# Kernel tuning notes

Measured on AMD Instinct MI355X. Metric: run time of the kernel, lower is better.

## Reference

```python
import jax, jax.numpy as jnp
import numpy as np

B, NX, NY, CIN = 4, 128, 128, 64
D, H = 64, 8  # out_channels, nhead
EPS = 1e-5


def setup_inputs() -> dict:
    key = jax.random.key(0)
    ks = jax.random.split(key, 12)
    s_in = 1.0 / np.sqrt(CIN)
    s_hd = 1.0 / np.sqrt(H * D)
    return {
        "v": jax.random.normal(ks[0], (B, NX, NY, CIN), jnp.float32),
        "Wq_w": jax.random.uniform(ks[1], (CIN, H * D), jnp.float32, -s_in, s_in),
        "Wq_b": jax.random.uniform(ks[2], (H * D,), jnp.float32, -s_in, s_in),
        "Wk_w": jax.random.uniform(ks[3], (CIN, H * D), jnp.float32, -s_in, s_in),
        "Wk_b": jax.random.uniform(ks[4], (H * D,), jnp.float32, -s_in, s_in),
        "Wv_w": jax.random.uniform(ks[5], (CIN, H * D), jnp.float32, -s_in, s_in),
        "Wv_b": jax.random.uniform(ks[6], (H * D,), jnp.float32, -s_in, s_in),
        "lnq_g": jnp.ones((H, D), jnp.float32),
        "lnq_b": jnp.zeros((H, D), jnp.float32),
        "lnk_g": jnp.ones((H, D), jnp.float32),
        "lnk_b": jnp.zeros((H, D), jnp.float32),
        "Wo_w": jax.random.uniform(ks[7], (H * D, D), jnp.float32, -s_hd, s_hd),
        "Wo_b": jax.random.uniform(ks[8], (D,), jnp.float32, -s_hd, s_hd),
    }


def _layernorm(x, gamma, beta):
    # x: [b,h,n,d]; gamma/beta: [h,d] (per-head params)
    mu = jnp.mean(x, axis=-1, keepdims=True)
    var = jnp.mean(jnp.square(x - mu), axis=-1, keepdims=True)
    xn = (x - mu) * jax.lax.rsqrt(var + EPS)
    return xn * gamma[None, :, None, :] + beta[None, :, None, :]


def reference(v, Wq_w, Wq_b, Wk_w, Wk_b, Wv_w, Wv_b,
              lnq_g, lnq_b, lnk_g, lnk_b, Wo_w, Wo_b):
    b, nx, ny, _ = v.shape
    n = nx * ny
    vf = v.reshape(b, n, -1)  # [b, n, cin]
    # QKV projections -> [b, h, n, d]
    def proj(w, bias):
        y = vf @ w + bias  # [b, n, h*d]
        return y.reshape(b, n, H, D).transpose(0, 2, 1, 3)
    Q = _layernorm(proj(Wq_w, Wq_b), lnq_g, lnq_b)
    K = _layernorm(proj(Wk_w, Wk_b), lnk_g, lnk_b)
    V = proj(Wv_w, Wv_b)
    # Non-softmax linear attention: (Q K^T) V == Q (K^T V); use O(n d^2) form
    kv = jnp.einsum('bhnd,bhne->bhde', K, V)      # [b,h,d,d]
    attn = jnp.einsum('bhmd,bhde->bhme', Q, kv)   # [b,h,n,d]
    attn = attn.transpose(0, 2, 1, 3).reshape(b, n, H * D)
    out = (attn @ Wo_w + Wo_b) / n
    return out.reshape(b, nx, ny, D)
```

## Files before the change

kernel.cpp:

```cpp
#include <hip/hip_runtime.h>
#include <hip/hip_bf16.h>

typedef __attribute__((ext_vector_type(8))) short bhalf8;
typedef __attribute__((ext_vector_type(4))) float f32x4;

#define MFMA_BF16 __builtin_amdgcn_mfma_f32_16x16x32_bf16

namespace {

constexpr int   NPIX  = 16384;
constexpr float EPSV  = 1e-5f;
constexpr float INV64 = 1.0f / 64.0f;
constexpr float INV_N = 1.0f / 16384.0f;

constexpr int KV1_OFF   = 0;
constexpr int T_OFF     = 131072;
constexpr int VSUM_OFF  = 131072 + 2048;
constexpr int CBETA_OFF = 131072 + 2048 + 256;
constexpr int FZERO_CNT = 131072 + 2048 + 256 + 256;

__device__ __host__ __forceinline__ unsigned short f2bf(float f) {
    unsigned int u = __builtin_bit_cast(unsigned int, f);
    u += 0x7fffu + ((u >> 16) & 1u);
    return (unsigned short)(u >> 16);
}

union B8 { bhalf8 v; unsigned int u[4]; ushort4 s4[2]; };

__device__ __forceinline__ unsigned int pk2(float a, float b) {
    union { __hip_bfloat162 h; unsigned int u; } x;
    x.h = __float22bfloat162_rn(float2{a, b});
    return x.u;
}

__global__ void k0_vsum(const float* __restrict__ v, float* __restrict__ vsum)
{
    const int blk = blockIdx.x, b = blockIdx.y, t = threadIdx.x;
    const int c4 = t & 15, p = t >> 4;
    float4 a = make_float4(0.f, 0.f, 0.f, 0.f);
    const float* base = v + ((size_t)b * NPIX + blk * 128) * 64 + c4 * 4;
#pragma unroll
    for (int i = 0; i < 8; ++i) {
        const float4 x = *reinterpret_cast<const float4*>(base + (size_t)(p * 8 + i) * 64);
        a.x += x.x; a.y += x.y; a.z += x.z; a.w += x.w;
    }
    __shared__ float4 red[16][16];
    red[p][c4] = a;
    __syncthreads();
    if (t < 16) {
        float4 s = red[0][t];
#pragma unroll
        for (int i = 1; i < 16; ++i) {
            const float4 x = red[i][t];
            s.x += x.x; s.y += x.y; s.z += x.z; s.w += x.w;
        }
        atomicAdd(vsum + b * 64 + t * 4 + 0, s.x);
        atomicAdd(vsum + b * 64 + t * 4 + 1, s.y);
        atomicAdd(vsum + b * 64 + t * 4 + 2, s.z);
        atomicAdd(vsum + b * 64 + t * 4 + 3, s.w);
    }
}

__global__ void kpack(const float* __restrict__ Wk, const float* __restrict__ Wv,
                      const float* __restrict__ Wq,
                      unsigned short* __restrict__ wkpk, unsigned short* __restrict__ wvpk,
                      unsigned short* __restrict__ wqpk, unsigned short* __restrict__ wksumb)
{
    const int w = blockIdx.x >> 3, h = blockIdx.x & 7, t = threadIdx.x;
    const float* W = (w == 0) ? Wk : (w == 1) ? Wv : Wq;
    unsigned short* dst = (w == 0) ? wkpk : (w == 1) ? wvpk : wqpk;

#pragma unroll
    for (int i = 0; i < 2; ++i) {
        const int f = t * 2 + i;
        const int nt = (f >> 7) & 3, ks = (f >> 6) & 1, l = f & 63;
        const int g = l >> 4, m = l & 15;
        ushort4 o0, o1;
        unsigned short tmp[8];
#pragma unroll
        for (int j = 0; j < 8; ++j)
            tmp[j] = f2bf(W[(size_t)(32 * ks + 8 * g + j) * 512 + h * 64 + 16 * nt + m]);
        o0 = make_ushort4(tmp[0], tmp[1], tmp[2], tmp[3]);
        o1 = make_ushort4(tmp[4], tmp[5], tmp[6], tmp[7]);
        unsigned short* d = dst + ((size_t)((h * 4 + nt) * 2 + ks)) * 512 + l * 8;
        *reinterpret_cast<ushort4*>(d)     = o0;
        *reinterpret_cast<ushort4*>(d + 4) = o1;
    }
    if (w == 0 && t < 64) {
        float s = 0.f;
        const float* row = Wk + (size_t)t * 512 + h * 64;
#pragma unroll
        for (int d = 0; d < 64; ++d) s += row[d];
        wksumb[h * 64 + t] = f2bf(s);
    }
}

__global__ __launch_bounds__(256, 2)
void k1_kv(const float* __restrict__ v,
           const unsigned short* __restrict__ wkpk, const unsigned short* __restrict__ wvpk,
           const unsigned short* __restrict__ wksumb,
           const float* __restrict__ bk, const float* __restrict__ bv,
           float* __restrict__ kv1, float* __restrict__ tG)
{
    const int ch = blockIdx.x, h = blockIdx.y, b = blockIdx.z;
    const int t = threadIdx.x, w = t >> 6, l = t & 63, g = l >> 4, m16 = l & 15;

    bhalf8 wkB[4][2], wvB[4][2], wks[2];
#pragma unroll
    for (int nt = 0; nt < 4; ++nt)
#pragma unroll
      for (int ks = 0; ks < 2; ++ks) {
          wkB[nt][ks] = *reinterpret_cast<const bhalf8*>(
              wkpk + ((size_t)((h * 4 + nt) * 2 + ks)) * 512 + l * 8);
          wvB[nt][ks] = *reinterpret_cast<const bhalf8*>(
              wvpk + ((size_t)((h * 4 + nt) * 2 + ks)) * 512 + l * 8);
      }
#pragma unroll
    for (int ks = 0; ks < 2; ++ks)
        wks[ks] = *reinterpret_cast<const bhalf8*>(wksumb + h * 64 + 32 * ks + 8 * g);

    float bksum;
    {
        float bl = bk[h * 64 + l];
#pragma unroll
        for (int m = 1; m < 64; m <<= 1) bl += __shfl_xor(bl, m, 64);
        bksum = bl;
    }
    float bkv[4], bvv[4];
#pragma unroll
    for (int nt = 0; nt < 4; ++nt) {
        bkv[nt] = bk[h * 64 + 16 * nt + m16];
        bvv[nt] = bv[h * 64 + 16 * nt + m16];
    }

    f32x4 kv[4][4];
#pragma unroll
    for (int i = 0; i < 4; ++i)
#pragma unroll
      for (int j = 0; j < 4; ++j) kv[i][j] = f32x4{0.f, 0.f, 0.f, 0.f};
    float tl[4] = {0.f, 0.f, 0.f, 0.f};

    const float* vw = v + ((size_t)b * NPIX + ch * 1024 + w * 256) * 64;

    for (int s = 0; s < 8; ++s) {
        B8 vA[2][2];
#pragma unroll
        for (int mt = 0; mt < 2; ++mt)
#pragma unroll
          for (int ks = 0; ks < 2; ++ks) {
              const float* src = vw + (size_t)(s * 32 + 16 * mt + m16) * 64 + 32 * ks + 8 * g;
              const float4 a = *reinterpret_cast<const float4*>(src);
              const float4 c = *reinterpret_cast<const float4*>(src + 4);
              vA[mt][ks].u[0] = pk2(a.x, a.y); vA[mt][ks].u[1] = pk2(a.z, a.w);
              vA[mt][ks].u[2] = pk2(c.x, c.y); vA[mt][ks].u[3] = pk2(c.z, c.w);
          }

        f32x4 kq[2][4];
#pragma unroll
        for (int mt = 0; mt < 2; ++mt)
#pragma unroll
          for (int nt = 0; nt < 4; ++nt) {
              f32x4 a = {0.f, 0.f, 0.f, 0.f};
              a = MFMA_BF16(vA[mt][0].v, wkB[nt][0], a, 0, 0, 0);
              a = MFMA_BF16(vA[mt][1].v, wkB[nt][1], a, 0, 0, 0);
#pragma unroll
              for (int q = 0; q < 4; ++q) a[q] += bkv[nt];
              kq[mt][nt] = a;
          }
        f32x4 st[2];
#pragma unroll
        for (int mt = 0; mt < 2; ++mt) {
            f32x4 a = {0.f, 0.f, 0.f, 0.f};
            a = MFMA_BF16(vA[mt][0].v, wks[0], a, 0, 0, 0);
            a = MFMA_BF16(vA[mt][1].v, wks[1], a, 0, 0, 0);
            st[mt] = a;
        }
        f32x4 s2p[2];
#pragma unroll
        for (int mt = 0; mt < 2; ++mt) {
#pragma unroll
            for (int q = 0; q < 4; ++q) {
                float acc = kq[mt][0][q] * kq[mt][0][q];
                acc = fmaf(kq[mt][1][q], kq[mt][1][q], acc);
                acc = fmaf(kq[mt][2][q], kq[mt][2][q], acc);
                acc = fmaf(kq[mt][3][q], kq[mt][3][q], acc);
                s2p[mt][q] = acc;
            }
        }
#pragma unroll
        for (int mt = 0; mt < 2; ++mt)
#pragma unroll
          for (int q = 0; q < 4; ++q) {
              float x = s2p[mt][q];
              x += __shfl_xor(x, 1, 64);
              x += __shfl_xor(x, 2, 64);
              x += __shfl_xor(x, 4, 64);
              x += __shfl_xor(x, 8, 64);
              s2p[mt][q] = x;
          }
        f32x4 rsv[2], cmu[2];
#pragma unroll
        for (int mt = 0; mt < 2; ++mt)
#pragma unroll
          for (int q = 0; q < 4; ++q) {
              const float mu  = (st[mt][q] + bksum) * INV64;
              const float var = s2p[mt][q] * INV64 - mu * mu;
              const float rs  = rsqrtf(fmaxf(var, 0.f) + EPSV);
              rsv[mt][q] = rs;
              cmu[mt][q] = mu * rs;
          }
        B8 ka[4];
#pragma unroll
        for (int MT = 0; MT < 4; ++MT) {
            ka[MT].u[0] = pk2(kq[0][MT][0] * rsv[0][0], kq[0][MT][1] * rsv[0][1]);
            ka[MT].u[1] = pk2(kq[0][MT][2] * rsv[0][2], kq[0][MT][3] * rsv[0][3]);
            ka[MT].u[2] = pk2(kq[1][MT][0] * rsv[1][0], kq[1][MT][1] * rsv[1][1]);
            ka[MT].u[3] = pk2(kq[1][MT][2] * rsv[1][2], kq[1][MT][3] * rsv[1][3]);
        }
        f32x4 vq[2][4];
#pragma unroll
        for (int mt = 0; mt < 2; ++mt)
#pragma unroll
          for (int nt = 0; nt < 4; ++nt) {
              f32x4 a = {0.f, 0.f, 0.f, 0.f};
              a = MFMA_BF16(vA[mt][0].v, wvB[nt][0], a, 0, 0, 0);
              a = MFMA_BF16(vA[mt][1].v, wvB[nt][1], a, 0, 0, 0);
#pragma unroll
              for (int q = 0; q < 4; ++q) a[q] += bvv[nt];
              vq[mt][nt] = a;
          }
#pragma unroll
        for (int nt = 0; nt < 4; ++nt) {
            float acc = tl[nt];
#pragma unroll
            for (int mt = 0; mt < 2; ++mt)
#pragma unroll
              for (int q = 0; q < 4; ++q)
                  acc = fmaf(cmu[mt][q], vq[mt][nt][q], acc);
            tl[nt] = acc;
        }
        B8 vb[4];
#pragma unroll
        for (int NT = 0; NT < 4; ++NT) {
            vb[NT].u[0] = pk2(vq[0][NT][0], vq[0][NT][1]);
            vb[NT].u[1] = pk2(vq[0][NT][2], vq[0][NT][3]);
            vb[NT].u[2] = pk2(vq[1][NT][0], vq[1][NT][1]);
            vb[NT].u[3] = pk2(vq[1][NT][2], vq[1][NT][3]);
        }
#pragma unroll
        for (int MT = 0; MT < 4; ++MT)
#pragma unroll
          for (int NT = 0; NT < 4; ++NT)
              kv[MT][NT] = MFMA_BF16(ka[MT].v, vb[NT].v, kv[MT][NT], 0, 0, 0);
    }

#pragma unroll
    for (int nt = 0; nt < 4; ++nt) {
        float x = tl[nt];
        x += __shfl_xor(x, 16, 64);
        x += __shfl_xor(x, 32, 64);
        tl[nt] = x;
    }
    if (g == 0) {
        float* td = tG + ((size_t)(b * 8 + h)) * 64;
#pragma unroll
        for (int nt = 0; nt < 4; ++nt) atomicAdd(td + 16 * nt + m16, tl[nt]);
    }

    __shared__ float kvred[4][4096];
    __syncthreads();
#pragma unroll
    for (int MT = 0; MT < 4; ++MT)
#pragma unroll
      for (int NT = 0; NT < 4; ++NT)
#pragma unroll
        for (int q = 0; q < 4; ++q)
            kvred[w][(16 * MT + 4 * g + q) * 64 + 16 * NT + m16] = kv[MT][NT][q];
    __syncthreads();
    float* dstg = kv1 + ((size_t)(b * 8 + h)) * 4096;
#pragma unroll
    for (int i = 0; i < 16; ++i) {
        const int idx = i * 256 + t;
        atomicAdd(dstg + idx,
                  kvred[0][idx] + kvred[1][idx] + kvred[2][idx] + kvred[3][idx]);
    }
}

__global__ void k2_mix(const float* __restrict__ kv1,  const float* __restrict__ tG,
                       const float* __restrict__ vsum,
                       const float* __restrict__ Wv,   const float* __restrict__ bv,
                       const float* __restrict__ lnkg, const float* __restrict__ lnkb,
                       const float* __restrict__ lnqg, const float* __restrict__ lnqb,
                       const float* __restrict__ Wo,   const float* __restrict__ Wob,
                       unsigned short* __restrict__ mpk, float* __restrict__ cbeta)
{
    const int h = blockIdx.x, b = blockIdx.y, t = threadIdx.x;
    __shared__ float kvs[64][65], wos[64][65], mls[64][65], Svs[64], us[64];
    const int r = t >> 2, c0 = (t & 3) * 16;
    const float* kg = kv1 + ((size_t)(b * 8 + h)) * 4096;
    const float* td = tG + ((size_t)(b * 8 + h)) * 64;
#pragma unroll
    for (int i = 0; i < 16; i += 4) {
        const float4 x = *reinterpret_cast<const float4*>(kg + r * 64 + c0 + i);
        kvs[r][c0+i] = x.x; kvs[r][c0+i+1] = x.y; kvs[r][c0+i+2] = x.z; kvs[r][c0+i+3] = x.w;
    }
#pragma unroll
    for (int i = 0; i < 16; i += 4) {
        const float4 x = *reinterpret_cast<const float4*>(Wo + ((size_t)(h * 64) + r) * 64 + c0 + i);
        wos[r][c0+i] = x.x; wos[r][c0+i+1] = x.y; wos[r][c0+i+2] = x.z; wos[r][c0+i+3] = x.w;
    }
    if (t < 64) {
        float s = 16384.f * bv[h * 64 + t];
        for (int cc = 0; cc < 64; ++cc)
            s = fmaf(vsum[b * 64 + cc], Wv[cc * 512 + h * 64 + t], s);
        Svs[t] = s;
    }
    __syncthreads();
    {
        const float gk = lnkg[h * 64 + r], bk2 = lnkb[h * 64 + r];
#pragma unroll
        for (int i = 0; i < 16; ++i) {
            const int e = c0 + i;
            kvs[r][e] = gk * (kvs[r][e] - td[e]) + bk2 * Svs[e];
        }
    }
    __syncthreads();
    if (t < 64) {
        float s = 0.f;
        for (int dd = 0; dd < 64; ++dd) s = fmaf(lnqb[h * 64 + dd], kvs[dd][t], s);
        us[t] = s;
    }
    float mrow[16];
#pragma unroll
    for (int i = 0; i < 16; ++i) mrow[i] = 0.f;
    for (int e2 = 0; e2 < 64; ++e2) {
        const float kr = kvs[r][e2];
#pragma unroll
        for (int i = 0; i < 16; ++i) mrow[i] = fmaf(kr, wos[e2][c0 + i], mrow[i]);
    }
    {
        const float gq = lnqg[h * 64 + r] * INV_N;
#pragma unroll
        for (int i = 0; i < 16; ++i) mls[r][c0 + i] = gq * mrow[i];
    }
    __syncthreads();
    if (t < 64) {
        float s = 0.f;
        for (int e2 = 0; e2 < 64; ++e2) s = fmaf(us[e2], wos[e2][t], s);
        atomicAdd(cbeta + b * 64 + t, s * INV_N);
        if (h == 0) atomicAdd(cbeta + b * 64 + t, Wob[t] * INV_N);
    }
#pragma unroll
    for (int i = 0; i < 2; ++i) {
        const int f = t * 2 + i;
        const int nt = (f >> 7) & 3, ks = (f >> 6) & 1, l = f & 63;
        const int g = l >> 4, m = l & 15;
        unsigned short o[8];
#pragma unroll
        for (int j = 0; j < 8; ++j) {
            const int d = 32 * ks + 16 * (j >> 2) + 4 * g + (j & 3);
            o[j] = f2bf(mls[d][16 * nt + m]);
        }
        unsigned short* dd = mpk + ((size_t)((b * 8 + h) * 8 + nt * 2 + ks)) * 512 + l * 8;
        *reinterpret_cast<ushort4*>(dd)     = make_ushort4(o[0], o[1], o[2], o[3]);
        *reinterpret_cast<ushort4*>(dd + 4) = make_ushort4(o[4], o[5], o[6], o[7]);
    }
}

__global__ __launch_bounds__(256, 2)
void k3_out(const float* __restrict__ v,
            const unsigned short* __restrict__ wqpk, const float* __restrict__ bq,
            const unsigned short* __restrict__ mpk,  const float* __restrict__ cbeta,
            float* __restrict__ out)
{
    const int blk = blockIdx.x, b = blockIdx.y;
    const int t = threadIdx.x, w = t >> 6, l = t & 63, g = l >> 4, m16 = l & 15;
    const size_t px0 = (size_t)b * NPIX + blk * 128 + w * 32;

    B8 vB[2][2];
#pragma unroll
    for (int nt = 0; nt < 2; ++nt)
#pragma unroll
      for (int ks = 0; ks < 2; ++ks) {
          const float* src = v + (px0 + 16 * nt + m16) * 64 + 32 * ks + 8 * g;
          const float4 a = *reinterpret_cast<const float4*>(src);
          const float4 c = *reinterpret_cast<const float4*>(src + 4);
          vB[nt][ks].u[0] = pk2(a.x, a.y); vB[nt][ks].u[1] = pk2(a.z, a.w);
          vB[nt][ks].u[2] = pk2(c.x, c.y); vB[nt][ks].u[3] = pk2(c.z, c.w);
      }
    float cbv[4];
#pragma unroll
    for (int nt = 0; nt < 4; ++nt) cbv[nt] = cbeta[b * 64 + 16 * nt + m16];

    f32x4 outa[2][4];
#pragma unroll
    for (int i = 0; i < 2; ++i)
#pragma unroll
      for (int j = 0; j < 4; ++j) outa[i][j] = f32x4{0.f, 0.f, 0.f, 0.f};

    for (int h = 0; h < 8; ++h) {
        bhalf8 wqA[4][2], mB[2][4];
#pragma unroll
        for (int mt = 0; mt < 4; ++mt)
#pragma unroll
          for (int ks = 0; ks < 2; ++ks)
            wqA[mt][ks] = *reinterpret_cast<const bhalf8*>(
                wqpk + ((size_t)((h * 4 + mt) * 2 + ks)) * 512 + l * 8);
#pragma unroll
        for (int ks = 0; ks < 2; ++ks)
#pragma unroll
          for (int nt = 0; nt < 4; ++nt)
            mB[ks][nt] = *reinterpret_cast<const bhalf8*>(
                mpk + ((size_t)((b * 8 + h) * 8 + nt * 2 + ks)) * 512 + l * 8);
        float4 bq4[4];
#pragma unroll
        for (int mt = 0; mt < 4; ++mt)
            bq4[mt] = *reinterpret_cast<const float4*>(bq + h * 64 + 16 * mt + 4 * g);

        f32x4 qa[4][2];
#pragma unroll
        for (int mt = 0; mt < 4; ++mt)
#pragma unroll
          for (int nt = 0; nt < 2; ++nt) {
              f32x4 a = {0.f, 0.f, 0.f, 0.f};
              a = MFMA_BF16(wqA[mt][0], vB[nt][0].v, a, 0, 0, 0);
              a = MFMA_BF16(wqA[mt][1], vB[nt][1].v, a, 0, 0, 0);
              a[0] += bq4[mt].x; a[1] += bq4[mt].y;
              a[2] += bq4[mt].z; a[3] += bq4[mt].w;
              qa[mt][nt] = a;
          }
        float mu[2], rs[2];
#pragma unroll
        for (int nt = 0; nt < 2; ++nt) {
            float s1 = 0.f, s2 = 0.f;
#pragma unroll
            for (int mt = 0; mt < 4; ++mt)
#pragma unroll
              for (int q = 0; q < 4; ++q) {
                  const float x = qa[mt][nt][q];
                  s1 += x; s2 = fmaf(x, x, s2);
              }
            s1 += __shfl_xor(s1, 16, 64); s1 += __shfl_xor(s1, 32, 64);
            s2 += __shfl_xor(s2, 16, 64); s2 += __shfl_xor(s2, 32, 64);
            mu[nt] = s1 * INV64;
            rs[nt] = rsqrtf(fmaxf(s2 * INV64 - mu[nt] * mu[nt], 0.f) + EPSV);
        }
        B8 ka[2][2];
#pragma unroll
        for (int MT = 0; MT < 2; ++MT)
#pragma unroll
          for (int ks = 0; ks < 2; ++ks) {
              ka[MT][ks].u[0] = pk2((qa[2*ks+0][MT][0] - mu[MT]) * rs[MT],
                                    (qa[2*ks+0][MT][1] - mu[MT]) * rs[MT]);
              ka[MT][ks].u[1] = pk2((qa[2*ks+0][MT][2] - mu[MT]) * rs[MT],
                                    (qa[2*ks+0][MT][3] - mu[MT]) * rs[MT]);
              ka[MT][ks].u[2] = pk2((qa[2*ks+1][MT][0] - mu[MT]) * rs[MT],
                                    (qa[2*ks+1][MT][1] - mu[MT]) * rs[MT]);
              ka[MT][ks].u[3] = pk2((qa[2*ks+1][MT][2] - mu[MT]) * rs[MT],
                                    (qa[2*ks+1][MT][3] - mu[MT]) * rs[MT]);
          }
#pragma unroll
        for (int MT = 0; MT < 2; ++MT)
#pragma unroll
          for (int nt = 0; nt < 4; ++nt) {
              outa[MT][nt] = MFMA_BF16(ka[MT][0].v, mB[0][nt], outa[MT][nt], 0, 0, 0);
              outa[MT][nt] = MFMA_BF16(ka[MT][1].v, mB[1][nt], outa[MT][nt], 0, 0, 0);
          }
    }

#pragma unroll
    for (int MT = 0; MT < 2; ++MT)
#pragma unroll
      for (int q = 0; q < 4; ++q) {
          float* orow = out + (px0 + 16 * MT + 4 * g + q) * 64;
#pragma unroll
          for (int nt = 0; nt < 4; ++nt)
              orow[16 * nt + m16] = outa[MT][nt][q] + cbv[nt];
      }
}

}

extern "C" void kernel_launch(void* const* d_in, const int* in_sizes, int n_in,
                              void* d_out, int out_size, void* d_ws, size_t ws_size,
                              hipStream_t stream)
{
    const float* v     = (const float*)d_in[0];
    const float* Wq_w  = (const float*)d_in[1];
    const float* Wq_b  = (const float*)d_in[2];
    const float* Wk_w  = (const float*)d_in[3];
    const float* Wk_b  = (const float*)d_in[4];
    const float* Wv_w  = (const float*)d_in[5];
    const float* Wv_b  = (const float*)d_in[6];
    const float* lnq_g = (const float*)d_in[7];
    const float* lnq_b = (const float*)d_in[8];
    const float* lnk_g = (const float*)d_in[9];
    const float* lnk_b = (const float*)d_in[10];
    const float* Wo_w  = (const float*)d_in[11];
    const float* Wo_b  = (const float*)d_in[12];
    float* out = (float*)d_out;

    float* wsf   = (float*)d_ws;
    float* kv1   = wsf + KV1_OFF;
    float* tG    = wsf + T_OFF;
    float* vsum  = wsf + VSUM_OFF;
    float* cbeta = wsf + CBETA_OFF;
    unsigned short* base_s = (unsigned short*)(wsf + FZERO_CNT);
    unsigned short* wkpk   = base_s;
    unsigned short* wvpk   = base_s + 32768;
    unsigned short* wqpk   = base_s + 65536;
    unsigned short* wksumb = base_s + 98304;
    unsigned short* mpk    = base_s + 98816;

    hipMemsetAsync(d_ws, 0, (size_t)FZERO_CNT * sizeof(float), stream);
    k0_vsum<<<dim3(128, 4), 256, 0, stream>>>(v, vsum);
    kpack<<<24, 256, 0, stream>>>(Wk_w, Wv_w, Wq_w, wkpk, wvpk, wqpk, wksumb);
    k1_kv<<<dim3(16, 8, 4), 256, 0, stream>>>(v, wkpk, wvpk, wksumb, Wk_b, Wv_b,
                                              kv1, tG);
    k2_mix<<<dim3(8, 4), 256, 0, stream>>>(kv1, tG, vsum, Wv_w, Wv_b,
                                           lnk_g, lnk_b, lnq_g, lnq_b,
                                           Wo_w, Wo_b, mpk, cbeta);
    k3_out<<<dim3(128, 4), 256, 0, stream>>>(v, wqpk, Wq_b, mpk, cbeta, out);
}
```

Baseline: 178.9 us.

## Share v tile across heads in LDS and replace atomics with two-stage reduction

The KV kernel now runs one 512-thread block per (chunk, batch), with each wave handling one head. It converts a 256-pixel tile of v to bf16 once into LDS instead of having every head re-read and re-convert v from global memory. Per-block partial kv/t/sum-of-V tiles are written to a workspace and reduced deterministically by a new reduce kernel plus the mix kernel. This removes the global atomics, the memset and the separate vsum kernel, since the V column sum is now accumulated in the KV pass. The cost is a larger workspace and extra global traffic for the partial tiles, plus one more launch.

```diff
diff --git a/kernel.cpp b/kernel.cpp
--- a/kernel.cpp
+++ b/kernel.cpp
@@ -9,23 +9,19 @@
 namespace {
 
 constexpr int   NPIX  = 16384;
+constexpr int   NCH   = 64;
+constexpr int   TILE  = 66 * 64;
 constexpr float EPSV  = 1e-5f;
 constexpr float INV64 = 1.0f / 64.0f;
 constexpr float INV_N = 1.0f / 16384.0f;
 
-constexpr int KV1_OFF   = 0;
-constexpr int T_OFF     = 131072;
-constexpr int VSUM_OFF  = 131072 + 2048;
-constexpr int CBETA_OFF = 131072 + 2048 + 256;
-constexpr int FZERO_CNT = 131072 + 2048 + 256 + 256;
-
-__device__ __host__ __forceinline__ unsigned short f2bf(float f) {
+__device__ __forceinline__ unsigned short f2bf(float f) {
     unsigned int u = __builtin_bit_cast(unsigned int, f);
     u += 0x7fffu + ((u >> 16) & 1u);
     return (unsigned short)(u >> 16);
 }
 
-union B8 { bhalf8 v; unsigned int u[4]; ushort4 s4[2]; };
+union B8 { bhalf8 v; unsigned int u[4]; };
 
 __device__ __forceinline__ unsigned int pk2(float a, float b) {
     union { __hip_bfloat162 h; unsigned int u; } x;
@@ -33,58 +29,30 @@
     return x.u;
 }
 
-__global__ void k0_vsum(const float* __restrict__ v, float* __restrict__ vsum)
-{
-    const int blk = blockIdx.x, b = blockIdx.y, t = threadIdx.x;
-    const int c4 = t & 15, p = t >> 4;
-    float4 a = make_float4(0.f, 0.f, 0.f, 0.f);
-    const float* base = v + ((size_t)b * NPIX + blk * 128) * 64 + c4 * 4;
-#pragma unroll
-    for (int i = 0; i < 8; ++i) {
-        const float4 x = *reinterpret_cast<const float4*>(base + (size_t)(p * 8 + i) * 64);
-        a.x += x.x; a.y += x.y; a.z += x.z; a.w += x.w;
-    }
-    __shared__ float4 red[16][16];
-    red[p][c4] = a;
-    __syncthreads();
-    if (t < 16) {
-        float4 s = red[0][t];
-#pragma unroll
-        for (int i = 1; i < 16; ++i) {
-            const float4 x = red[i][t];
-            s.x += x.x; s.y += x.y; s.z += x.z; s.w += x.w;
-        }
-        atomicAdd(vsum + b * 64 + t * 4 + 0, s.x);
-        atomicAdd(vsum + b * 64 + t * 4 + 1, s.y);
-        atomicAdd(vsum + b * 64 + t * 4 + 2, s.z);
-        atomicAdd(vsum + b * 64 + t * 4 + 3, s.w);
-    }
-}
-
 __global__ void kpack(const float* __restrict__ Wk, const float* __restrict__ Wv,
                       const float* __restrict__ Wq,
                       unsigned short* __restrict__ wkpk, unsigned short* __restrict__ wvpk,
-                      unsigned short* __restrict__ wqpk, unsigned short* __restrict__ wksumb)
+                      unsigned short* __restrict__ wqpk, unsigned short* __restrict__ wksumb,
+                      float* __restrict__ cbeta)
 {
     const int w = blockIdx.x >> 3, h = blockIdx.x & 7, t = threadIdx.x;
     const float* W = (w == 0) ? Wk : (w == 1) ? Wv : Wq;
     unsigned short* dst = (w == 0) ? wkpk : (w == 1) ? wvpk : wqpk;
 
+    if (blockIdx.x == 0) cbeta[t] = 0.f;
+
 #pragma unroll
     for (int i = 0; i < 2; ++i) {
         const int f = t * 2 + i;
         const int nt = (f >> 7) & 3, ks = (f >> 6) & 1, l = f & 63;
         const int g = l >> 4, m = l & 15;
-        ushort4 o0, o1;
         unsigned short tmp[8];
 #pragma unroll
         for (int j = 0; j < 8; ++j)
             tmp[j] = f2bf(W[(size_t)(32 * ks + 8 * g + j) * 512 + h * 64 + 16 * nt + m]);
-        o0 = make_ushort4(tmp[0], tmp[1], tmp[2], tmp[3]);
-        o1 = make_ushort4(tmp[4], tmp[5], tmp[6], tmp[7]);
         unsigned short* d = dst + ((size_t)((h * 4 + nt) * 2 + ks)) * 512 + l * 8;
-        *reinterpret_cast<ushort4*>(d)     = o0;
-        *reinterpret_cast<ushort4*>(d + 4) = o1;
+        *reinterpret_cast<ushort4*>(d)     = make_ushort4(tmp[0], tmp[1], tmp[2], tmp[3]);
+        *reinterpret_cast<ushort4*>(d + 4) = make_ushort4(tmp[4], tmp[5], tmp[6], tmp[7]);
     }
     if (w == 0 && t < 64) {
         float s = 0.f;
@@ -95,15 +63,30 @@
     }
 }
 
-__global__ __launch_bounds__(256, 2)
-void k1_kv(const float* __restrict__ v,
+__global__ __launch_bounds__(512, 2)
+void ka_kv(const float* __restrict__ v,
            const unsigned short* __restrict__ wkpk, const unsigned short* __restrict__ wvpk,
            const unsigned short* __restrict__ wksumb,
            const float* __restrict__ bk, const float* __restrict__ bv,
-           float* __restrict__ kv1, float* __restrict__ tG)
+           float* __restrict__ part)
 {
-    const int ch = blockIdx.x, h = blockIdx.y, b = blockIdx.z;
-    const int t = threadIdx.x, w = t >> 6, l = t & 63, g = l >> 4, m16 = l & 15;
+    const int ch = blockIdx.x, b = blockIdx.y;
+    const int t = threadIdx.x, h = t >> 6, l = t & 63, g = l >> 4, m16 = l & 15;
+
+    __shared__ uint4 vlds4[2048];
+    unsigned short* vlds = reinterpret_cast<unsigned short*>(vlds4);
+
+    const float* vbase = v + ((size_t)b * NPIX + ch * 256) * 64;
+#pragma unroll
+    for (int i = 0; i < 4; ++i) {
+        const int G = t + 512 * i;
+        const int s = G >> 8, f = (G >> 6) & 3, ll = G & 63;
+        const int mt = f >> 1, ks = f & 1, gg = ll >> 4, mm = ll & 15;
+        const float* src = vbase + (size_t)(s * 32 + 16 * mt + mm) * 64 + 32 * ks + 8 * gg;
+        const float4 a = *reinterpret_cast<const float4*>(src);
+        const float4 c = *reinterpret_cast<const float4*>(src + 4);
+        vlds4[G] = uint4{pk2(a.x, a.y), pk2(a.z, a.w), pk2(c.x, c.y), pk2(c.z, c.w)};
+    }
 
     bhalf8 wkB[4][2], wvB[4][2], wks[2];
 #pragma unroll
@@ -139,21 +122,18 @@
 #pragma unroll
       for (int j = 0; j < 4; ++j) kv[i][j] = f32x4{0.f, 0.f, 0.f, 0.f};
     float tl[4] = {0.f, 0.f, 0.f, 0.f};
-
-    const float* vw = v + ((size_t)b * NPIX + ch * 1024 + w * 256) * 64;
+    float sv[4] = {0.f, 0.f, 0.f, 0.f};
+
+    __syncthreads();
 
     for (int s = 0; s < 8; ++s) {
-        B8 vA[2][2];
+        bhalf8 vA[2][2];
 #pragma unroll
         for (int mt = 0; mt < 2; ++mt)
 #pragma unroll
-          for (int ks = 0; ks < 2; ++ks) {
-              const float* src = vw + (size_t)(s * 32 + 16 * mt + m16) * 64 + 32 * ks + 8 * g;
-              const float4 a = *reinterpret_cast<const float4*>(src);
-              const float4 c = *reinterpret_cast<const float4*>(src + 4);
-              vA[mt][ks].u[0] = pk2(a.x, a.y); vA[mt][ks].u[1] = pk2(a.z, a.w);
-              vA[mt][ks].u[2] = pk2(c.x, c.y); vA[mt][ks].u[3] = pk2(c.z, c.w);
-          }
+          for (int ks = 0; ks < 2; ++ks)
+            vA[mt][ks] = *reinterpret_cast<const bhalf8*>(
+                vlds + ((size_t)(s * 4 + mt * 2 + ks) * 64 + l) * 8);
 
         f32x4 kq[2][4];
 #pragma unroll
@@ -161,8 +141,8 @@
 #pragma unroll
           for (int nt = 0; nt < 4; ++nt) {
               f32x4 a = {0.f, 0.f, 0.f, 0.f};
-              a = MFMA_BF16(vA[mt][0].v, wkB[nt][0], a, 0, 0, 0);
-              a = MFMA_BF16(vA[mt][1].v, wkB[nt][1], a, 0, 0, 0);
+              a = MFMA_BF16(vA[mt][0], wkB[nt][0], a, 0, 0, 0);
+              a = MFMA_BF16(vA[mt][1], wkB[nt][1], a, 0, 0, 0);
 #pragma unroll
               for (int q = 0; q < 4; ++q) a[q] += bkv[nt];
               kq[mt][nt] = a;
@@ -171,22 +151,21 @@
 #pragma unroll
         for (int mt = 0; mt < 2; ++mt) {
             f32x4 a = {0.f, 0.f, 0.f, 0.f};
-            a = MFMA_BF16(vA[mt][0].v, wks[0], a, 0, 0, 0);
-            a = MFMA_BF16(vA[mt][1].v, wks[1], a, 0, 0, 0);
+            a = MFMA_BF16(vA[mt][0], wks[0], a, 0, 0, 0);
+            a = MFMA_BF16(vA[mt][1], wks[1], a, 0, 0, 0);
             st[mt] = a;
         }
         f32x4 s2p[2];
 #pragma unroll
-        for (int mt = 0; mt < 2; ++mt) {
-#pragma unroll
-            for (int q = 0; q < 4; ++q) {
-                float acc = kq[mt][0][q] * kq[mt][0][q];
-                acc = fmaf(kq[mt][1][q], kq[mt][1][q], acc);
-                acc = fmaf(kq[mt][2][q], kq[mt][2][q], acc);
-                acc = fmaf(kq[mt][3][q], kq[mt][3][q], acc);
-                s2p[mt][q] = acc;
-            }
-        }
+        for (int mt = 0; mt < 2; ++mt)
+#pragma unroll
+          for (int q = 0; q < 4; ++q) {
+              float acc = kq[mt][0][q] * kq[mt][0][q];
+              acc = fmaf(kq[mt][1][q], kq[mt][1][q], acc);
+              acc = fmaf(kq[mt][2][q], kq[mt][2][q], acc);
+              acc = fmaf(kq[mt][3][q], kq[mt][3][q], acc);
+              s2p[mt][q] = acc;
+          }
 #pragma unroll
         for (int mt = 0; mt < 2; ++mt)
 #pragma unroll
@@ -223,21 +202,23 @@
 #pragma unroll
           for (int nt = 0; nt < 4; ++nt) {
               f32x4 a = {0.f, 0.f, 0.f, 0.f};
-              a = MFMA_BF16(vA[mt][0].v, wvB[nt][0], a, 0, 0, 0);
-              a = MFMA_BF16(vA[mt][1].v, wvB[nt][1], a, 0, 0, 0);
+              a = MFMA_BF16(vA[mt][0], wvB[nt][0], a, 0, 0, 0);
+              a = MFMA_BF16(vA[mt][1], wvB[nt][1], a, 0, 0, 0);
 #pragma unroll
               for (int q = 0; q < 4; ++q) a[q] += bvv[nt];
               vq[mt][nt] = a;
           }
 #pragma unroll
         for (int nt = 0; nt < 4; ++nt) {
-            float acc = tl[nt];
+            float acc = tl[nt], acc2 = sv[nt];
 #pragma unroll
             for (int mt = 0; mt < 2; ++mt)
 #pragma unroll
-              for (int q = 0; q < 4; ++q)
-                  acc = fmaf(cmu[mt][q], vq[mt][nt][q], acc);
-            tl[nt] = acc;
+              for (int q = 0; q < 4; ++q) {
+                  acc  = fmaf(cmu[mt][q], vq[mt][nt][q], acc);
+                  acc2 += vq[mt][nt][q];
+              }
+            tl[nt] = acc; sv[nt] = acc2;
         }
         B8 vb[4];
 #pragma unroll
@@ -257,63 +238,91 @@
 #pragma unroll
     for (int nt = 0; nt < 4; ++nt) {
         float x = tl[nt];
-        x += __shfl_xor(x, 16, 64);
-        x += __shfl_xor(x, 32, 64);
+        x += __shfl_xor(x, 16, 64); x += __shfl_xor(x, 32, 64);
         tl[nt] = x;
-    }
+        float y = sv[nt];
+        y += __shfl_xor(y, 16, 64); y += __shfl_xor(y, 32, 64);
+        sv[nt] = y;
+    }
+    float* pdst = part + ((size_t)((b * NCH + ch) * 8 + h)) * TILE;
+#pragma unroll
+    for (int MT = 0; MT < 4; ++MT)
+#pragma unroll
+      for (int NT = 0; NT < 4; ++NT)
+#pragma unroll
+        for (int q = 0; q < 4; ++q)
+            pdst[(16 * MT + 4 * g + q) * 64 + 16 * NT + m16] = kv[MT][NT][q];
     if (g == 0) {
-        float* td = tG + ((size_t)(b * 8 + h)) * 64;
-#pragma unroll
-        for (int nt = 0; nt < 4; ++nt) atomicAdd(td + 16 * nt + m16, tl[nt]);
-    }
-
-    __shared__ float kvred[4][4096];
-    __syncthreads();
-#pragma unroll
-    for (int MT = 0; MT < 4; ++MT)
-#pragma unroll
-      for (int NT = 0; NT < 4; ++NT)
-#pragma unroll
-        for (int q = 0; q < 4; ++q)
-            kvred[w][(16 * MT + 4 * g + q) * 64 + 16 * NT + m16] = kv[MT][NT][q];
-    __syncthreads();
-    float* dstg = kv1 + ((size_t)(b * 8 + h)) * 4096;
-#pragma unroll
-    for (int i = 0; i < 16; ++i) {
-        const int idx = i * 256 + t;
-        atomicAdd(dstg + idx,
-                  kvred[0][idx] + kvred[1][idx] + kvred[2][idx] + kvred[3][idx]);
-    }
-}
-
-__global__ void k2_mix(const float* __restrict__ kv1,  const float* __restrict__ tG,
-                       const float* __restrict__ vsum,
-                       const float* __restrict__ Wv,   const float* __restrict__ bv,
-                       const float* __restrict__ lnkg, const float* __restrict__ lnkb,
-                       const float* __restrict__ lnqg, const float* __restrict__ lnqb,
-                       const float* __restrict__ Wo,   const float* __restrict__ Wob,
-                       unsigned short* __restrict__ mpk, float* __restrict__ cbeta)
+#pragma unroll
+        for (int nt = 0; nt < 4; ++nt) {
+            pdst[64 * 64 + 16 * nt + m16] = tl[nt];
+            pdst[65 * 64 + 16 * nt + m16] = sv[nt];
+        }
+    }
+}
+
+__global__ void k2a_reduce(const float* __restrict__ part, float* __restrict__ s2buf)
+{
+    const int seg = blockIdx.x, bh = blockIdx.y, t = threadIdx.x;
+    const int b = bh >> 3, hh = bh & 7;
+    const float* base = part + ((size_t)((b * NCH + seg * 8) * 8 + hh)) * TILE;
+    float* dst = s2buf + ((size_t)(bh * 8 + seg)) * TILE;
+#pragma unroll
+    for (int k = 0; k < 5; ++k) {
+        const int idx = t + k * 256;
+        if (idx < TILE / 4) {
+            float4 s = make_float4(0.f, 0.f, 0.f, 0.f);
+#pragma unroll
+            for (int i = 0; i < 8; ++i) {
+                const float4 x = *reinterpret_cast<const float4*>(
+                    base + (size_t)i * 8 * TILE + idx * 4);
+                s.x += x.x; s.y += x.y; s.z += x.z; s.w += x.w;
+            }
+            *reinterpret_cast<float4*>(dst + idx * 4) = s;
+        }
+    }
+}
+
+__global__ void k2b_mix(const float* __restrict__ s2buf,
+                        const float* __restrict__ lnkg, const float* __restrict__ lnkb,
+                        const float* __restrict__ lnqg, const float* __restrict__ lnqb,
+                        const float* __restrict__ Wo,   const float* __restrict__ Wob,
+                        unsigned short* __restrict__ mpk, float* __restrict__ cbeta)
 {
     const int h = blockIdx.x, b = blockIdx.y, t = threadIdx.x;
-    __shared__ float kvs[64][65], wos[64][65], mls[64][65], Svs[64], us[64];
+    __shared__ float kvs[64][65], wos[64][65], mls[64][65], Svs[64], tds[64], us[64];
     const int r = t >> 2, c0 = (t & 3) * 16;
-    const float* kg = kv1 + ((size_t)(b * 8 + h)) * 4096;
-    const float* td = tG + ((size_t)(b * 8 + h)) * 64;
+    const float* sb = s2buf + ((size_t)((b * 8 + h) * 8)) * TILE;
+
+    float acc[16];
+#pragma unroll
+    for (int i = 0; i < 16; ++i) acc[i] = 0.f;
+#pragma unroll
+    for (int seg = 0; seg < 8; ++seg) {
+        const float* src = sb + (size_t)seg * TILE + r * 64 + c0;
+#pragma unroll
+        for (int q = 0; q < 4; ++q) {
+            const float4 x = *reinterpret_cast<const float4*>(src + 4 * q);
+            acc[4*q+0] += x.x; acc[4*q+1] += x.y; acc[4*q+2] += x.z; acc[4*q+3] += x.w;
+        }
+    }
+#pragma unroll
+    for (int i = 0; i < 16; ++i) kvs[r][c0 + i] = acc[i];
+
+    if (t < 64) {
+        float s = 0.f, s2 = 0.f;
+#pragma unroll
+        for (int seg = 0; seg < 8; ++seg) {
+            s  += sb[(size_t)seg * TILE + 64 * 64 + t];
+            s2 += sb[(size_t)seg * TILE + 65 * 64 + t];
+        }
+        tds[t] = s; Svs[t] = s2;
+    }
 #pragma unroll
     for (int i = 0; i < 16; i += 4) {
-        const float4 x = *reinterpret_cast<const float4*>(kg + r * 64 + c0 + i);
-        kvs[r][c0+i] = x.x; kvs[r][c0+i+1] = x.y; kvs[r][c0+i+2] = x.z; kvs[r][c0+i+3] = x.w;
-    }
-#pragma unroll
-    for (int i = 0; i < 16; i += 4) {
-        const float4 x = *reinterpret_cast<const float4*>(Wo + ((size_t)(h * 64) + r) * 64 + c0 + i);
+        const float4 x = *reinterpret_cast<const float4*>(
+            Wo + ((size_t)(h * 64) + r) * 64 + c0 + i);
         wos[r][c0+i] = x.x; wos[r][c0+i+1] = x.y; wos[r][c0+i+2] = x.z; wos[r][c0+i+3] = x.w;
-    }
-    if (t < 64) {
-        float s = 16384.f * bv[h * 64 + t];
-        for (int cc = 0; cc < 64; ++cc)
-            s = fmaf(vsum[b * 64 + cc], Wv[cc * 512 + h * 64 + t], s);
-        Svs[t] = s;
     }
     __syncthreads();
     {
@@ -321,7 +330,7 @@
 #pragma unroll
         for (int i = 0; i < 16; ++i) {
             const int e = c0 + i;
-            kvs[r][e] = gk * (kvs[r][e] - td[e]) + bk2 * Svs[e];
+            kvs[r][e] = gk * (kvs[r][e] - tds[e]) + bk2 * Svs[e];
         }
     }
     __syncthreads();
@@ -398,6 +407,7 @@
 #pragma unroll
       for (int j = 0; j < 4; ++j) outa[i][j] = f32x4{0.f, 0.f, 0.f, 0.f};
 
+#pragma unroll
     for (int h = 0; h < 8; ++h) {
         bhalf8 wqA[4][2], mB[2][4];
 #pragma unroll
@@ -500,25 +510,21 @@
     const float* Wo_b  = (const float*)d_in[12];
     float* out = (float*)d_out;
 
-    float* wsf   = (float*)d_ws;
-    float* kv1   = wsf + KV1_OFF;
-    float* tG    = wsf + T_OFF;
-    float* vsum  = wsf + VSUM_OFF;
-    float* cbeta = wsf + CBETA_OFF;
-    unsigned short* base_s = (unsigned short*)(wsf + FZERO_CNT);
+    float* wsf    = (float*)d_ws;
+    float* part   = wsf;
+    float* s2buf  = part + (size_t)4 * NCH * 8 * TILE;
+    float* cbeta  = s2buf + (size_t)32 * 8 * TILE;
+    unsigned short* base_s = (unsigned short*)(cbeta + 256);
     unsigned short* wkpk   = base_s;
     unsigned short* wvpk   = base_s + 32768;
     unsigned short* wqpk   = base_s + 65536;
     unsigned short* wksumb = base_s + 98304;
     unsigned short* mpk    = base_s + 98816;
 
-    hipMemsetAsync(d_ws, 0, (size_t)FZERO_CNT * sizeof(float), stream);
-    k0_vsum<<<dim3(128, 4), 256, 0, stream>>>(v, vsum);
-    kpack<<<24, 256, 0, stream>>>(Wk_w, Wv_w, Wq_w, wkpk, wvpk, wqpk, wksumb);
-    k1_kv<<<dim3(16, 8, 4), 256, 0, stream>>>(v, wkpk, wvpk, wksumb, Wk_b, Wv_b,
-                                              kv1, tG);
-    k2_mix<<<dim3(8, 4), 256, 0, stream>>>(kv1, tG, vsum, Wv_w, Wv_b,
-                                           lnk_g, lnk_b, lnq_g, lnq_b,
-                                           Wo_w, Wo_b, mpk, cbeta);
+    kpack<<<24, 256, 0, stream>>>(Wk_w, Wv_w, Wq_w, wkpk, wvpk, wqpk, wksumb, cbeta);
+    ka_kv<<<dim3(NCH, 4), 512, 0, stream>>>(v, wkpk, wvpk, wksumb, Wk_b, Wv_b, part);
+    k2a_reduce<<<dim3(8, 32), 256, 0, stream>>>(part, s2buf);
+    k2b_mix<<<dim3(8, 4), 256, 0, stream>>>(s2buf, lnk_g, lnk_b, lnq_g, lnq_b,
+                                            Wo_w, Wo_b, mpk, cbeta);
     k3_out<<<dim3(128, 4), 256, 0, stream>>>(v, wqpk, Wq_b, mpk, cbeta, out);
 }
```

Result: faster. 161.3 us (-9.8%).
